# Kernel tuning notes

Measured on AMD Instinct MI355X. Metric: run time of the kernel, lower is better.

## Reference

```python
import jax, jax.numpy as jnp
import numpy as np

D_MODEL = 256
NUM_HEADS = 8
DEPTH = D_MODEL // NUM_HEADS
CITY_SEQ = 2048
B = 4
SQ = 2048
EPS = 1e-9
WEIGHTING = 'IDW'  # branch used (Linear/IDW/Gaussian in original)


def setup_inputs() -> dict:
    key = jax.random.key(0)
    ks = jax.random.split(key, 12)
    s = 1.0 / np.sqrt(D_MODEL)
    return {
        'query': jax.random.normal(ks[0], (B, SQ, D_MODEL), jnp.float32),
        'values': jax.random.normal(ks[1], (B, SQ, D_MODEL), jnp.float32),
        'distance_matrix': jax.random.uniform(ks[2], (B, SQ, CITY_SEQ), jnp.float32),
        'Wq_w': jax.random.normal(ks[3], (D_MODEL, D_MODEL), jnp.float32) * s,
        'Wq_b': jnp.zeros((D_MODEL,), jnp.float32),
        'Wk_w': jax.random.normal(ks[4], (D_MODEL, D_MODEL), jnp.float32) * s,
        'Wk_b': jnp.zeros((D_MODEL,), jnp.float32),
        'Wv_w': jax.random.normal(ks[5], (D_MODEL, D_MODEL), jnp.float32) * s,
        'Wv_b': jnp.zeros((D_MODEL,), jnp.float32),
        'fc_w': jax.random.normal(ks[6], (D_MODEL, D_MODEL), jnp.float32) * s,
        'fc_b': jnp.zeros((D_MODEL,), jnp.float32),
        'trainable_keys': jax.random.normal(ks[7], (CITY_SEQ, D_MODEL), jnp.float32),
    }


def _distance_weights(dist):
    # IDW branch: per-row normalized inverse distance, shape [B, Sq, S]
    inv = 1.0 / (dist + EPS)
    return inv / jnp.sum(inv, axis=-1, keepdims=True)


def reference(query, values, distance_matrix, Wq_w, Wq_b, Wk_w, Wk_b,
              Wv_w, Wv_b, fc_w, fc_b, trainable_keys):
    b = query.shape[0]
    q = query @ Wq_w.T + Wq_b                      # [B, Sq, D]
    k = trainable_keys @ Wk_w.T + Wk_b             # [S, D] (shared across batch)
    v = values @ Wv_w.T + Wv_b                     # [B, S, D]

    qh = q.reshape(b, -1, NUM_HEADS, DEPTH)        # [B, Sq, H, d]
    kh = k.reshape(-1, NUM_HEADS, DEPTH)           # [S, H, d]
    vh = v.reshape(b, -1, NUM_HEADS, DEPTH)        # [B, S, H, d]

    scale = 1.0 / jnp.sqrt(jnp.asarray(DEPTH, jnp.float32))
    scores = jnp.einsum('bqhd,khd->bhqk', qh, kh) * scale   # [B, H, Sq, S]
    dw = _distance_weights(distance_matrix)[:, None, :, :]  # [B, 1, Sq, S]
    scores = scores * dw
    attn = jax.nn.softmax(scores, axis=-1)
    out = jnp.einsum('bhqk,bkhd->bqhd', attn, vh).reshape(b, -1, D_MODEL)
    return out @ fc_w.T + fc_b
```

## Files before the change

### kernel.cpp

```cpp
#include <hip/hip_runtime.h>

#define BB 4
#define SQn 2048
#define SS 2048
#define DM 256
#define DH 32

typedef unsigned short u16;
typedef unsigned int u32;
typedef _Float16 f16;
typedef __attribute__((ext_vector_type(8))) f16 f16x8;
typedef __attribute__((ext_vector_type(8))) short s16x8;
typedef __attribute__((ext_vector_type(4))) float f32x4;
typedef __attribute__((ext_vector_type(2))) float f32x2;
typedef __attribute__((ext_vector_type(4))) u32 u32x4;
typedef __attribute__((ext_vector_type(2))) u32 u32x2;

__device__ __forceinline__ float bf2f(u16 x){ u32 u=((u32)x)<<16; return __builtin_bit_cast(float,u); }
__device__ __forceinline__ u16 f2bf(float f){ u32 u=__builtin_bit_cast(u32,f); u32 r=(u+0x7fffu+((u>>16)&1u))>>16; return (u16)r; }

__device__ __forceinline__ f16x8 ld8(const void* p, size_t off, int fl)
{
    f16x8 r;
    if (fl) {
        const float* f = (const float*)p + off;
        f32x4 a = *(const f32x4*)f;
        f32x4 b = *(const f32x4*)(f + 4);
        #pragma unroll
        for (int i = 0; i < 4; ++i) { r[i] = (f16)a[i]; r[4+i] = (f16)b[i]; }
    } else {
        const u16* s = (const u16*)p + off;
        u32x4 v = *(const u32x4*)s;
        #pragma unroll
        for (int i = 0; i < 4; ++i) {
            u32 x = v[i];
            r[2*i]   = (f16)bf2f((u16)(x & 0xffff));
            r[2*i+1] = (f16)bf2f((u16)(x >> 16));
        }
    }
    return r;
}
__device__ __forceinline__ float ld1(const void* p, int idx, int fl)
{ return fl ? ((const float*)p)[idx] : bf2f(((const u16*)p)[idx]); }

__device__ __forceinline__ f32x2 ld_d2(const void* p, int fl, size_t off)
{
    f32x2 r;
    if (fl) r = *(const f32x2*)((const float*)p + off);
    else {
        u32 x = *(const u32*)((const u16*)p + off);
        r[0] = bf2f((u16)(x & 0xffff)); r[1] = bf2f((u16)(x >> 16));
    }
    return r;
}

__global__ void detect_kernel(const u32* __restrict__ q, int* __restrict__ flag)
{
    int t = threadIdx.x;
    u32 w = q[t];
    u32 e = (w >> 7) & 0xFFu;
    int vote = ((e >= 0x70u && e <= 0x85u) || ((w & 0xFFFFu) == 0u)) ? 1 : 0;
    #pragma unroll
    for (int d = 1; d < 64; d <<= 1) vote += __shfl_xor(vote, d);
    __shared__ int ps[4];
    if ((t & 63) == 0) ps[t >> 6] = vote;
    __syncthreads();
    if (t == 0) *flag = ((ps[0]+ps[1]+ps[2]+ps[3]) >= 128) ? 0 : 1;
}

__global__ __launch_bounds__(256) void proj_kernel(
    const int* __restrict__ flag,
    const void* __restrict__ query, const void* __restrict__ values, const void* __restrict__ tkeys,
    const void* __restrict__ Wq, const void* __restrict__ Wqb,
    const void* __restrict__ Wk, const void* __restrict__ Wkb,
    const void* __restrict__ Wv, const void* __restrict__ Wvb,
    f16* __restrict__ qf, f16* __restrict__ kf, u16* __restrict__ vt)
{
    int fl = *flag;
    int bx = blockIdx.x;
    const void *X, *W, *Bi; int mode, rowbase;
    if (bx < 128)      { X=query;  W=Wq; Bi=Wqb; mode=0; rowbase=bx*64; }
    else if (bx < 256) { X=values; W=Wv; Bi=Wvb; mode=2; rowbase=(bx-128)*64; }
    else               { X=tkeys;  W=Wk; Bi=Wkb; mode=1; rowbase=(bx-256)*64; }
    int colbase = blockIdx.y * 64;

    __shared__ f16 Xs[64][40];
    __shared__ f16 Ws[64][40];
    __shared__ u16 Os[64][72];

    int t = threadIdx.x;
    int lane = t & 63, w = t >> 6;
    int quad = lane >> 4, l15 = lane & 15;

    const f32x4 fz = {0.f,0.f,0.f,0.f};
    f32x4 acc[4] = {fz,fz,fz,fz};

    for (int ks = 0; ks < 8; ++ks) {
        int k0 = ks * 32;
        {
            int row = t >> 2, ch = (t & 3) * 8;
            f16x8 xv = ld8(X, (size_t)(rowbase+row)*DM + k0 + ch, fl);
            f16x8 wv = ld8(W, (size_t)(colbase+row)*DM + k0 + ch, fl);
            *(f16x8*)(&Xs[row][ch]) = xv;
            *(f16x8*)(&Ws[row][ch]) = wv;
        }
        __syncthreads();
        f16x8 a = *(const f16x8*)(&Xs[w*16 + l15][quad*8]);
        #pragma unroll
        for (int nt = 0; nt < 4; ++nt) {
            f16x8 bfr = *(const f16x8*)(&Ws[nt*16 + l15][quad*8]);
            acc[nt] = __builtin_amdgcn_mfma_f32_16x16x32_f16(a, bfr, acc[nt], 0, 0, 0);
        }
        __syncthreads();
    }

    if (mode == 2) {
        int m = rowbase + w*16 + quad*4;
        int bb = m >> 11, s = m & 2047;
        int ktv = s >> 5, qv = (s >> 3) & 3, kk = s & 7;
        #pragma unroll
        for (int nt = 0; nt < 4; ++nt) {
            int col = colbase + nt*16 + l15;
            float bv = ld1(Bi, col, fl);
            int hv = col >> 5, ntv = (col >> 4) & 1;
            size_t idx = (((((size_t)(bb*8 + hv))*64 + ktv)*2 + ntv)*4 + qv)*128
                         + (size_t)(col & 15)*8 + kk;
            u32x2 pk;
            pk[0] = (u32)f2bf(acc[nt][0]+bv) | ((u32)f2bf(acc[nt][1]+bv) << 16);
            pk[1] = (u32)f2bf(acc[nt][2]+bv) | ((u32)f2bf(acc[nt][3]+bv) << 16);
            *(u32x2*)(vt + idx) = pk;
        }
    } else {
        #pragma unroll
        for (int nt = 0; nt < 4; ++nt) {
            int col = nt*16 + l15;
            float bv = ld1(Bi, colbase + col, fl);
            #pragma unroll
            for (int r = 0; r < 4; ++r)
                Os[w*16 + quad*4 + r][col] = __builtin_bit_cast(u16, (f16)(acc[nt][r] + bv));
        }
        __syncthreads();
        #pragma unroll
        for (int p = 0; p < 2; ++p) {
            int rr = (t >> 3) + p*32;
            int ch = (t & 7) * 8;
            u32x4 v = *(const u32x4*)(&Os[rr][ch]);
            if (mode == 0) {
                *(u32x4*)(qf + (size_t)(rowbase+rr)*DM + colbase + ch) = v;
            } else {
                int head = (colbase + ch) >> 5;
                int dh = ch & 31;
                *(u32x4*)(kf + (size_t)head*(SS*DH) + (size_t)(rowbase+rr)*DH + dh) = v;
            }
        }
    }
}

__global__ __launch_bounds__(256) void dwsum_kernel(
    const int* __restrict__ flag, const void* __restrict__ dist, float* __restrict__ rs)
{
    int fl = *flag;
    int row = blockIdx.x;
    int t = threadIdx.x;
    float s = 0.f;
    if (fl) {
        const float* p = (const float*)dist + (size_t)row * SS + t*8;
        f32x4 a = *(const f32x4*)p;
        f32x4 b = *(const f32x4*)(p + 4);
        #pragma unroll
        for (int i = 0; i < 4; ++i) { s += 1.0f/(a[i]+1e-9f); s += 1.0f/(b[i]+1e-9f); }
    } else {
        const u16* p = (const u16*)dist + (size_t)row * SS + t*8;
        u32x4 v = *(const u32x4*)p;
        #pragma unroll
        for (int i = 0; i < 4; ++i) {
            u32 x = v[i];
            s += 1.0f / (bf2f((u16)(x & 0xffff)) + 1e-9f);
            s += 1.0f / (bf2f((u16)(x >> 16))    + 1e-9f);
        }
    }
    #pragma unroll
    for (int d = 1; d < 64; d <<= 1) s += __shfl_xor(s, d);
    __shared__ float ps[4];
    if ((t & 63) == 0) ps[t >> 6] = s;
    __syncthreads();
    if (t == 0) rs[row] = 0.17677669529663687f / (ps[0] + ps[1] + ps[2] + ps[3]);
}

#define LDP 40
#define LDO 264
#define DB_OFF 40960
#define DB_LD 36
#define OL_OFF  49152
#define OUTF_OFF 66048

__global__ __launch_bounds__(1024) void attn_kernel(
    const int* __restrict__ flag,
    const void* __restrict__ dist, const float* __restrict__ rs,
    const f16* __restrict__ qf, const f16* __restrict__ kf, const u16* __restrict__ vtg,
    const void* __restrict__ fcw, const void* __restrict__ fcb,
    void* __restrict__ out)
{
    __shared__ __align__(16) char smem[99840];

    int fl = *flag;
    int t = threadIdx.x;
    int w = t >> 6, lane = t & 63;
    int quad = lane >> 4, l15 = lane & 15;
    int b = blockIdx.y, q0 = blockIdx.x * 32;
    int h = w & 7, khalf = w >> 3;

    u16* Pw = (u16*)(smem + w * 2560);
    float* dbB = (float*)(smem + DB_OFF);

    float rsq[2];
    rsq[0] = rs[b*SQn + q0 + l15];
    rsq[1] = rs[b*SQn + q0 + 16 + l15];

    f16x8 aq[2];
    #pragma unroll
    for (int mt = 0; mt < 2; ++mt)
        aq[mt] = *(const f16x8*)(qf + (size_t)(b*SQn + q0 + mt*16 + l15)*DM + h*DH + quad*8);

    u32 ov = (l15 == 0) ? 0x3F803F80u : 0u;
    u32x4 ovv = {ov, ov, ov, ov};
    s16x8 ones = __builtin_bit_cast(s16x8, ovv);

    const f32x4 fz = {0.f,0.f,0.f,0.f};
    f32x4 o[2][2] = {{fz,fz},{fz,fz}};
    f32x4 lacc[2] = {fz, fz};

    const f16* kfh = kf + (size_t)h * (SS*DH);
    const u16* vth = vtg + (((size_t)(b*8 + h)) << 16);

    int g  = t >> 9;
    int tt = t & 511;
    int srow = tt >> 4, scol = (tt & 15) * 2;
    size_t dbase = (size_t)(b*SQn + q0 + srow)*SS + g*1024 + scol;
    int drw = srow*DB_LD + scol;

    {
        f32x2 sv = ld_d2(dist, fl, dbase);
        float* d0 = dbB + g*1152;
        d0[drw] = sv[0]; d0[drw+1] = sv[1];
    }
    f16x8 ck[2]; s16x8 cv[2];
    {
        int ktg0 = khalf * 32;
        #pragma unroll
        for (int nt = 0; nt < 2; ++nt) {
            ck[nt] = *(const f16x8*)(kfh + (size_t)(ktg0*32 + nt*16 + l15)*DH + quad*8);
            cv[nt] = __builtin_bit_cast(s16x8,
                *(const u32x4*)(vth + (size_t)ktg0*1024 + nt*512 + quad*128 + l15*8));
        }
    }
    __syncthreads();

    for (int kt = 0; kt < 32; ++kt) {
        int ktn  = (kt + 1) & 31;
        int ktgn = khalf*32 + ktn;

        f32x2 sv = ld_d2(dist, fl, dbase + (size_t)ktn*32);
        f16x8 nk[2]; s16x8 nv[2];
        #pragma unroll
        for (int nt = 0; nt < 2; ++nt) {
            nk[nt] = *(const f16x8*)(kfh + (size_t)(ktgn*32 + nt*16 + l15)*DH + quad*8);
            nv[nt] = __builtin_bit_cast(s16x8,
                *(const u32x4*)(vth + (size_t)ktgn*1024 + nt*512 + quad*128 + l15*8));
        }

        const float* dbc = dbB + ((kt & 1)*2 + khalf)*1152;
        f32x4 dd[2][2];
        #pragma unroll
        for (int mt = 0; mt < 2; ++mt)
            #pragma unroll
            for (int nt = 0; nt < 2; ++nt)
                dd[mt][nt] = *(const f32x4*)(dbc + (mt*16 + l15)*DB_LD + nt*16 + quad*4);

        f32x4 st[2][2];
        #pragma unroll
        for (int mt = 0; mt < 2; ++mt)
            #pragma unroll
            for (int nt = 0; nt < 2; ++nt)
                st[mt][nt] = __builtin_amdgcn_mfma_f32_16x16x32_f16(ck[nt], aq[mt], fz, 0, 0, 0);

        #pragma unroll
        for (int mt = 0; mt < 2; ++mt)
            #pragma unroll
            for (int nt = 0; nt < 2; ++nt) {
                f32x4 d = dd[mt][nt];
                u32 pb[4];
                #pragma unroll
                for (int r = 0; r < 4; ++r) {
                    float dwv = rsq[mt] * __builtin_amdgcn_rcpf(d[r] + 1e-9f);
                    float p = __expf(st[mt][nt][r] * dwv);
                    pb[r] = __builtin_bit_cast(u32, p);
                }
                u32x2 pk;
                pk[0] = __builtin_amdgcn_perm(pb[1], pb[0], 0x07060302u);
                pk[1] = __builtin_amdgcn_perm(pb[3], pb[2], 0x07060302u);
                *(u32x2*)(Pw + (mt*16 + l15)*LDP + nt*16 + quad*4) = pk;
            }
        __asm__ __volatile__("" ::: "memory");

        #pragma unroll
        for (int mt = 0; mt < 2; ++mt) {
            s16x8 ap = *(const s16x8*)(Pw + (mt*16 + l15)*LDP + quad*8);
            lacc[mt] = __builtin_amdgcn_mfma_f32_16x16x32_bf16(ap, ones, lacc[mt], 0, 0, 0);
            #pragma unroll
            for (int nt = 0; nt < 2; ++nt)
                o[mt][nt] = __builtin_amdgcn_mfma_f32_16x16x32_bf16(ap, cv[nt], o[mt][nt], 0, 0, 0);
        }

        {
            float* dbn = dbB + (((kt + 1) & 1)*2 + g)*1152;
            dbn[drw] = sv[0]; dbn[drw+1] = sv[1];
        }
        __syncthreads();

        ck[0] = nk[0]; ck[1] = nk[1]; cv[0] = nv[0]; cv[1] = nv[1];
    }

    float* Cx = (float*)smem;
    if (w >= 8) {
        float* dst = Cx + ((w - 8)*64 + lane)*24;
        *(f32x4*)(dst +  0) = o[0][0];
        *(f32x4*)(dst +  4) = o[0][1];
        *(f32x4*)(dst +  8) = o[1][0];
        *(f32x4*)(dst + 12) = o[1][1];
        *(f32x4*)(dst + 16) = lacc[0];
        *(f32x4*)(dst + 20) = lacc[1];
    }
    __syncthreads();
    f16* Ol = (f16*)(smem + OL_OFF);
    if (w < 8) {
        const float* src = Cx + (w*64 + lane)*24;
        o[0][0] += *(const f32x4*)(src +  0);
        o[0][1] += *(const f32x4*)(src +  4);
        o[1][0] += *(const f32x4*)(src +  8);
        o[1][1] += *(const f32x4*)(src + 12);
        lacc[0] += *(const f32x4*)(src + 16);
        lacc[1] += *(const f32x4*)(src + 20);

        #pragma unroll
        for (int mt = 0; mt < 2; ++mt)
            #pragma unroll
            for (int r = 0; r < 4; ++r) {
                float lv = __shfl(lacc[mt][r], lane & 48);
                float inv = 1.0f / lv;
                o[mt][0][r] *= inv;
                o[mt][1][r] *= inv;
            }

        #pragma unroll
        for (int mt = 0; mt < 2; ++mt)
            #pragma unroll
            for (int nt = 0; nt < 2; ++nt)
                #pragma unroll
                for (int r = 0; r < 4; ++r)
                    Ol[(mt*16 + quad*4 + r)*LDO + h*DH + nt*16 + l15] = (f16)o[mt][nt][r];
    }
    __syncthreads();

    f32x4 c[2] = {fz, fz};
    int n = w*16 + l15;
    for (int ks = 0; ks < 8; ++ks) {
        f16x8 bw = ld8(fcw, (size_t)n*DM + ks*32 + quad*8, fl);
        #pragma unroll
        for (int mt = 0; mt < 2; ++mt) {
            f16x8 a2 = *(const f16x8*)(Ol + (mt*16 + l15)*LDO + ks*32 + quad*8);
            c[mt] = __builtin_amdgcn_mfma_f32_16x16x32_f16(a2, bw, c[mt], 0, 0, 0);
        }
    }
    float* OutF = (float*)(smem + OUTF_OFF);
    {
        float bv = ld1(fcb, n, fl);
        #pragma unroll
        for (int mt = 0; mt < 2; ++mt)
            #pragma unroll
            for (int r = 0; r < 4; ++r)
                OutF[(mt*16 + quad*4 + r)*LDO + n] = c[mt][r] + bv;
    }
    __syncthreads();
    if (fl) {
        float* of = (float*)out;
        int row = t >> 5, col = (t & 31) * 8;
        f32x4 v0 = *(const f32x4*)(OutF + row*LDO + col);
        f32x4 v1 = *(const f32x4*)(OutF + row*LDO + col + 4);
        float* dst = of + ((size_t)(b*SQn + q0 + row))*DM + col;
        *(f32x4*)dst       = v0;
        *(f32x4*)(dst + 4) = v1;
    } else {
        u16* ob = (u16*)out;
        int row = t >> 5, col = (t & 31) * 8;
        f32x4 v0 = *(const f32x4*)(OutF + row*LDO + col);
        f32x4 v1 = *(const f32x4*)(OutF + row*LDO + col + 4);
        u32x4 pk;
        pk[0] = (u32)f2bf(v0[0]) | ((u32)f2bf(v0[1]) << 16);
        pk[1] = (u32)f2bf(v0[2]) | ((u32)f2bf(v0[3]) << 16);
        pk[2] = (u32)f2bf(v1[0]) | ((u32)f2bf(v1[1]) << 16);
        pk[3] = (u32)f2bf(v1[2]) | ((u32)f2bf(v1[3]) << 16);
        *(u32x4*)(ob + ((size_t)(b*SQn + q0 + row))*DM + col) = pk;
    }
}

extern "C" void kernel_launch(void* const* d_in, const int* in_sizes, int n_in,
                              void* d_out, int out_size, void* d_ws, size_t ws_size,
                              hipStream_t stream)
{
    const void* query  = d_in[0];
    const void* values = d_in[1];
    const void* dist   = d_in[2];
    const void* Wq     = d_in[3];
    const void* Wqb    = d_in[4];
    const void* Wk     = d_in[5];
    const void* Wkb    = d_in[6];
    const void* Wv     = d_in[7];
    const void* Wvb    = d_in[8];
    const void* fcw    = d_in[9];
    const void* fcb    = d_in[10];
    const void* tkeys  = d_in[11];

    char* ws   = (char*)d_ws;
    f16*  qf   = (f16*)ws;
    f16*  kf   = (f16*)(ws + (4u << 20));
    u16*  vt   = (u16*)(ws + (5u << 20));
    float* rsp = (float*)(ws + (9u << 20));
    int*  flag = (int*)(ws + (9u << 20) + 32768);

    detect_kernel<<<1, 256, 0, stream>>>((const u32*)query, flag);
    proj_kernel<<<dim3(288, 4), 256, 0, stream>>>(flag, query, values, tkeys,
                                                  Wq, Wqb, Wk, Wkb, Wv, Wvb,
                                                  qf, kf, vt);
    dwsum_kernel<<<dim3(BB * SQn), 256, 0, stream>>>(flag, dist, rsp);
    attn_kernel<<<dim3(64, 4), 1024, 0, stream>>>(flag, dist, rsp, qf, kf, vt, fcw, fcb, d_out);
}
```

Before: 196.5 us.

## Precompute normalized distance weights in MFMA fragment layout for attention

The row-sum kernel now also computes the full normalized, scaled inverse-distance weight for every element and writes it to a workspace buffer in the exact per-lane MFMA fragment order. The attention kernel loads these weights with contiguous vector reads instead of strided raw distances, and drops its per-element reciprocal and row-scale multiply. The cost is an extra 64 MB fp32 write and read through global memory, since the distance matrix is effectively read twice (raw, then transformed), along with an added block barrier in the prepass.

```diff
diff --git a/kernel.cpp b/kernel.cpp
--- a/kernel.cpp
+++ b/kernel.cpp
@@ -42,17 +42,6 @@
 }
 __device__ __forceinline__ float ld1(const void* p, int idx, int fl)
 { return fl ? ((const float*)p)[idx] : bf2f(((const u16*)p)[idx]); }
-
-__device__ __forceinline__ f32x2 ld_d2(const void* p, int fl, size_t off)
-{
-    f32x2 r;
-    if (fl) r = *(const f32x2*)((const float*)p + off);
-    else {
-        u32 x = *(const u32*)((const u16*)p + off);
-        r[0] = bf2f((u16)(x & 0xffff)); r[1] = bf2f((u16)(x >> 16));
-    }
-    return r;
-}
 
 __global__ void detect_kernel(const u32* __restrict__ q, int* __restrict__ flag)
 {
@@ -157,46 +146,67 @@
 }
 
 __global__ __launch_bounds__(256) void dwsum_kernel(
-    const int* __restrict__ flag, const void* __restrict__ dist, float* __restrict__ rs)
+    const int* __restrict__ flag, const void* __restrict__ dist, float* __restrict__ distT)
 {
     int fl = *flag;
     int row = blockIdx.x;
     int t = threadIdx.x;
-    float s = 0.f;
+
+    float d[8];
     if (fl) {
         const float* p = (const float*)dist + (size_t)row * SS + t*8;
         f32x4 a = *(const f32x4*)p;
-        f32x4 b = *(const f32x4*)(p + 4);
-        #pragma unroll
-        for (int i = 0; i < 4; ++i) { s += 1.0f/(a[i]+1e-9f); s += 1.0f/(b[i]+1e-9f); }
+        f32x4 b4 = *(const f32x4*)(p + 4);
+        #pragma unroll
+        for (int i = 0; i < 4; ++i) { d[i] = a[i]; d[4+i] = b4[i]; }
     } else {
         const u16* p = (const u16*)dist + (size_t)row * SS + t*8;
         u32x4 v = *(const u32x4*)p;
         #pragma unroll
         for (int i = 0; i < 4; ++i) {
             u32 x = v[i];
-            s += 1.0f / (bf2f((u16)(x & 0xffff)) + 1e-9f);
-            s += 1.0f / (bf2f((u16)(x >> 16))    + 1e-9f);
-        }
-    }
+            d[2*i]   = bf2f((u16)(x & 0xffff));
+            d[2*i+1] = bf2f((u16)(x >> 16));
+        }
+    }
+    float s = 0.f;
     #pragma unroll
-    for (int d = 1; d < 64; d <<= 1) s += __shfl_xor(s, d);
+    for (int i = 0; i < 8; ++i) s += 1.0f / (d[i] + 1e-9f);
+    #pragma unroll
+    for (int dd = 1; dd < 64; dd <<= 1) s += __shfl_xor(s, dd);
     __shared__ float ps[4];
+    __shared__ float srs;
     if ((t & 63) == 0) ps[t >> 6] = s;
     __syncthreads();
-    if (t == 0) rs[row] = 0.17677669529663687f / (ps[0] + ps[1] + ps[2] + ps[3]);
+    if (t == 0) srs = 0.17677669529663687f / (ps[0] + ps[1] + ps[2] + ps[3]);
+    __syncthreads();
+    float rs = srs;
+
+    int b = row >> 11, q = row & 2047;
+    int qt = q >> 5, mt = (q >> 4) & 1, l15 = q & 15;
+    #pragma unroll
+    for (int c = 0; c < 2; ++c) {
+        int k = t*8 + c*4;
+        int kt = k >> 5, nt = (k >> 4) & 1, quad = (k >> 2) & 3;
+        f32x4 wv;
+        #pragma unroll
+        for (int r = 0; r < 4; ++r)
+            wv[r] = rs * __builtin_amdgcn_rcpf(d[c*4 + r] + 1e-9f);
+        size_t idx = ((size_t)((b*64 + qt)*64 + kt))*1024
+                     + (mt*2 + nt)*256 + (quad*16 + l15)*4;
+        *(f32x4*)(distT + idx) = wv;
+    }
 }
 
 #define LDP 40
 #define LDO 264
 #define DB_OFF 40960
-#define DB_LD 36
 #define OL_OFF  49152
 #define OUTF_OFF 66048
 
 __global__ __launch_bounds__(1024) void attn_kernel(
     const int* __restrict__ flag,
-    const void* __restrict__ dist, const float* __restrict__ rs,
+    const float* __restrict__ distT,
     const f16* __restrict__ qf, const f16* __restrict__ kf, const u16* __restrict__ vtg,
     const void* __restrict__ fcw, const void* __restrict__ fcb,
     void* __restrict__ out)
@@ -213,10 +223,6 @@
     u16* Pw = (u16*)(smem + w * 2560);
     float* dbB = (float*)(smem + DB_OFF);
 
-    float rsq[2];
-    rsq[0] = rs[b*SQn + q0 + l15];
-    rsq[1] = rs[b*SQn + q0 + 16 + l15];
-
     f16x8 aq[2];
     #pragma unroll
     for (int mt = 0; mt < 2; ++mt)
@@ -232,17 +238,15 @@
 
     const f16* kfh = kf + (size_t)h * (SS*DH);
     const u16* vth = vtg + (((size_t)(b*8 + h)) << 16);
+    const float* dTb = distT + ((size_t)(b*64 + blockIdx.x))*64*1024;
 
     int g  = t >> 9;
     int tt = t & 511;
-    int srow = tt >> 4, scol = (tt & 15) * 2;
-    size_t dbase = (size_t)(b*SQn + q0 + srow)*SS + g*1024 + scol;
-    int drw = srow*DB_LD + scol;
 
     {
-        f32x2 sv = ld_d2(dist, fl, dbase);
-        float* d0 = dbB + g*1152;
-        d0[drw] = sv[0]; d0[drw+1] = sv[1];
+        f32x2 sv = *(const f32x2*)(dTb + (size_t)(g*32)*1024 + tt*2);
+        float* d0 = dbB + g*1024;
+        *(f32x2*)(d0 + tt*2) = sv;
     }
     f16x8 ck[2]; s16x8 cv[2];
     {
@@ -260,7 +264,7 @@
         int ktn  = (kt + 1) & 31;
         int ktgn = khalf*32 + ktn;
 
-        f32x2 sv = ld_d2(dist, fl, dbase + (size_t)ktn*32);
+        f32x2 sv = *(const f32x2*)(dTb + (size_t)(g*32 + ktn)*1024 + tt*2);
         f16x8 nk[2]; s16x8 nv[2];
         #pragma unroll
         for (int nt = 0; nt < 2; ++nt) {
@@ -269,13 +273,13 @@
                 *(const u32x4*)(vth + (size_t)ktgn*1024 + nt*512 + quad*128 + l15*8));
         }
 
-        const float* dbc = dbB + ((kt & 1)*2 + khalf)*1152;
+        const float* dbc = dbB + ((kt & 1)*2 + khalf)*1024;
         f32x4 dd[2][2];
         #pragma unroll
         for (int mt = 0; mt < 2; ++mt)
             #pragma unroll
             for (int nt = 0; nt < 2; ++nt)
-                dd[mt][nt] = *(const f32x4*)(dbc + (mt*16 + l15)*DB_LD + nt*16 + quad*4);
+                dd[mt][nt] = *(const f32x4*)(dbc + (mt*2 + nt)*256 + lane*4);
 
         f32x4 st[2][2];
         #pragma unroll
@@ -288,12 +292,10 @@
         for (int mt = 0; mt < 2; ++mt)
             #pragma unroll
             for (int nt = 0; nt < 2; ++nt) {
-                f32x4 d = dd[mt][nt];
                 u32 pb[4];
                 #pragma unroll
                 for (int r = 0; r < 4; ++r) {
-                    float dwv = rsq[mt] * __builtin_amdgcn_rcpf(d[r] + 1e-9f);
-                    float p = __expf(st[mt][nt][r] * dwv);
+                    float p = __expf(st[mt][nt][r] * dd[mt][nt][r]);
                     pb[r] = __builtin_bit_cast(u32, p);
                 }
                 u32x2 pk;
@@ -313,8 +315,8 @@
         }
 
         {
-            float* dbn = dbB + (((kt + 1) & 1)*2 + g)*1152;
-            dbn[drw] = sv[0]; dbn[drw+1] = sv[1];
+            float* dbn = dbB + (((kt + 1) & 1)*2 + g)*1024;
+            *(f32x2*)(dbn + tt*2) = sv;
         }
         __syncthreads();
 
@@ -425,13 +427,13 @@
     f16*  qf   = (f16*)ws;
     f16*  kf   = (f16*)(ws + (4u << 20));
     u16*  vt   = (u16*)(ws + (5u << 20));
-    float* rsp = (float*)(ws + (9u << 20));
-    int*  flag = (int*)(ws + (9u << 20) + 32768);
+    int*  flag = (int*)(ws + (9u << 20));
+    float* dT  = (float*)(ws + (16u << 20));
 
     detect_kernel<<<1, 256, 0, stream>>>((const u32*)query, flag);
     proj_kernel<<<dim3(288, 4), 256, 0, stream>>>(flag, query, values, tkeys,
                                                   Wq, Wqb, Wk, Wkb, Wv, Wvb,
                                                   qf, kf, vt);
-    dwsum_kernel<<<dim3(BB * SQn), 256, 0, stream>>>(flag, dist, rsp);
-    attn_kernel<<<dim3(64, 4), 1024, 0, stream>>>(flag, dist, rsp, qf, kf, vt, fcw, fcb, d_out);
-}
+    dwsum_kernel<<<dim3(BB * SQn), 256, 0, stream>>>(flag, dist, dT);
+    attn_kernel<<<dim3(64, 4), 1024, 0, stream>>>(flag, dT, qf, kf, vt, fcw, fcb, d_out);
+}
```

New measurement: 236.0 us. +20.1%, slower.
